# Optimization experiments

Measured on AMD Instinct MI355X. Metric: run time of the kernel, lower is better.

## Reference

```python
import jax, jax.numpy as jnp
import numpy as np

BS, T, ND, DS = 512, 100, 10, 6
INS, HID = 256, 256
CAT = INS * ND + HID  # 2816


def setup_inputs() -> dict:
    key = jax.random.key(0)
    ks = jax.random.split(key, 12)
    s = 0.02
    return {
        "descriptors": jax.random.normal(ks[0], (BS, T, ND, DS), jnp.float32),
        "Wd": jax.random.normal(ks[1], (INS, DS), jnp.float32) * s,
        "bd": jnp.zeros((INS,), jnp.float32),
        "W1": jax.random.normal(ks[2], (CAT, CAT), jnp.float32) * s,
        "b1": jnp.zeros((CAT,), jnp.float32),
        "W2": jax.random.normal(ks[3], (HID, CAT), jnp.float32) * s,
        "b2": jnp.zeros((HID,), jnp.float32),
        "Wv": jax.random.normal(ks[4], (ND, CAT), jnp.float32) * s,
        "bv": jnp.zeros((ND,), jnp.float32),
        "Wih": jax.random.normal(ks[5], (4 * HID, INS), jnp.float32) * s,
        "Whh": jax.random.normal(ks[6], (4 * HID, HID), jnp.float32) * s,
        "bih": jnp.zeros((4 * HID,), jnp.float32),
        "bhh": jnp.zeros((4 * HID,), jnp.float32),
    }


def reference(descriptors, Wd, bd, W1, b1, W2, b2, Wv, bv, Wih, Whh, bih, bhh):
    bs = descriptors.shape[0]
    # project all descriptors at once (same math as per-step Linear)
    emb = jnp.einsum('btnd,id->btni', descriptors, Wd) + bd  # [bs,T,ND,INS]
    emb = emb.reshape(bs, T, ND * INS).transpose(1, 0, 2)    # [T,bs,ND*INS]

    h0 = jnp.zeros((bs, HID), jnp.float32)
    c0 = jnp.zeros((bs, HID), jnp.float32)
    x0 = jnp.zeros((bs, HID), jnp.float32)  # lstm_in_size == hidden_size

    def step(carry, emb_t):
        h, c, inp = carry
        gates = inp @ Wih.T + bih + h @ Whh.T + bhh  # [bs,4*HID]
        i, f, g, o = jnp.split(gates, 4, axis=-1)
        c = jax.nn.sigmoid(f) * c + jax.nn.sigmoid(i) * jnp.tanh(g)
        h = jax.nn.sigmoid(o) * jnp.tanh(c)
        x = jnp.concatenate([emb_t, h], axis=-1)     # [bs,CAT]
        z = jax.nn.relu(x @ W1.T + b1)
        nxt = jax.nn.relu(z @ W2.T + b2)
        a = jax.nn.sigmoid(z @ Wv.T + bv)            # eval mode -> sigmoid
        return (h, c, nxt), a

    _, att = jax.lax.scan(step, (h0, c0, x0), emb)   # [T,bs,ND]
    return att.transpose(1, 0, 2)                    # [bs,T,ND]
```

## Files before the change

### kernel.cpp

```cpp
#include <hip/hip_runtime.h>
#include <math.h>

#define BSZ 512
#define TT  100
#define NDD 10
#define DSS 6
#define INS 256
#define HID 256
#define CAT 2816
#define KZ  320
#define NOUTP 320
#define NOUT 266
#define NBLK 256
#define NTHR 1024

typedef short sh8 __attribute__((ext_vector_type(8)));
typedef float f4  __attribute__((ext_vector_type(4)));
typedef unsigned int u4 __attribute__((ext_vector_type(4)));
typedef unsigned short ushort_t;

__device__ __forceinline__ float sigf(float x) { return 1.0f / (1.0f + expf(-x)); }

__device__ __forceinline__ ushort_t f2bf(float f) {
    union { float f; unsigned int u; } v; v.f = f;
    unsigned int r = (v.u + 0x7FFFu + ((v.u >> 16) & 1u)) >> 16;
    return (ushort_t)r;
}

#define MFMA(a, b, c) __builtin_amdgcn_mfma_f32_16x16x32_bf16((a), (b), (c), 0, 0, 0)
#define ALOAD(p)    __hip_atomic_load((p), __ATOMIC_RELAXED, __HIP_MEMORY_SCOPE_AGENT)
#define ASTORE(p,v) __hip_atomic_store((p), (v), __ATOMIC_RELAXED, __HIP_MEMORY_SCOPE_AGENT)

__device__ __forceinline__ u4 aload16(const unsigned int* p) {
    u4 r;
    asm volatile("global_load_dwordx4 %0, %1, off sc0 sc1\n\ts_waitcnt vmcnt(0)"
                 : "=&v"(r) : "v"(p) : "memory");
    return r;
}
__device__ __forceinline__ void aload16x4(f4* a, const float* p0, const float* p1,
                                          const float* p2, const float* p3) {
    asm volatile(
        "global_load_dwordx4 %0, %4, off sc0 sc1\n\t"
        "global_load_dwordx4 %1, %5, off sc0 sc1\n\t"
        "global_load_dwordx4 %2, %6, off sc0 sc1\n\t"
        "global_load_dwordx4 %3, %7, off sc0 sc1\n\t"
        "s_waitcnt vmcnt(0)"
        : "=&v"(a[0]), "=&v"(a[1]), "=&v"(a[2]), "=&v"(a[3])
        : "v"(p0), "v"(p1), "v"(p2), "v"(p3)
        : "memory");
}

__global__ __launch_bounds__(64) void k_fold(
    const float* __restrict__ W1, const float* __restrict__ Wd,
    const float* __restrict__ bd, const float* __restrict__ b1,
    ushort_t* __restrict__ Wzc, float* __restrict__ bfold)
{
    __shared__ float sW1[2560];
    __shared__ float sWd[INS * DSS];
    __shared__ float red[64];
    const int j = blockIdx.x;
    const int tid = threadIdx.x;
    for (int f = tid; f < INS * DSS; f += 64) sWd[f] = Wd[f];
    for (int f = tid; f < 2560; f += 64) sW1[f] = W1[(size_t)j * CAT + f];
    __syncthreads();
    if (tid < 60) {
        int n = tid / DSS, d = tid - n * DSS;
        float acc = 0.f;
        for (int i = 0; i < INS; ++i) acc += sW1[n * INS + i] * sWd[i * DSS + d];
        Wzc[j * KZ + tid] = f2bf(acc);
    } else {
        Wzc[j * KZ + tid] = 0;
    }
    for (int q = tid; q < HID; q += 64)
        Wzc[j * KZ + 64 + q] = f2bf(W1[(size_t)j * CAT + 2560 + q]);
    float acc = 0.f;
    for (int p = tid; p < 2560; p += 64) acc += sW1[p] * bd[p & (INS - 1)];
    red[tid] = acc;
    __syncthreads();
    for (int s = 32; s > 0; s >>= 1) {
        if (tid < s) red[tid] += red[tid + s];
        __syncthreads();
    }
    if (tid == 0) bfold[j] = b1[j] + red[0];
}

__global__ __launch_bounds__(256) void k_dfold(
    const float* __restrict__ desc, ushort_t* __restrict__ Dfold)
{
    int idx = blockIdx.x * 256 + threadIdx.x;
    int p = idx & 63;
    int tb = idx >> 6;
    int t = tb / BSZ;
    int b = tb - t * BSZ;
    float v = (p < 60) ? desc[(size_t)b * (TT * 60) + t * 60 + p] : 0.f;
    Dfold[idx] = f2bf(v);
}

__global__ __launch_bounds__(256) void k_prep_g(
    const float* __restrict__ Wih, const float* __restrict__ Whh,
    const float* __restrict__ bih, const float* __restrict__ bhh,
    ushort_t* __restrict__ Wg, float* __restrict__ bg)
{
    int idx = blockIdx.x * 256 + threadIdx.x;
    int newr = idx >> 9, k = idx & 511;
    int j = newr >> 2, g = newr & 3;
    int src_row = g * 256 + j;
    float v = (k < 256) ? Wih[(size_t)src_row * INS + k]
                        : Whh[(size_t)src_row * HID + (k - 256)];
    Wg[idx] = f2bf(v);
    if (k == 0) bg[newr] = bih[src_row] + bhh[src_row];
}

__global__ __launch_bounds__(256) void k_prep_o(
    const float* __restrict__ W2, const float* __restrict__ Wv,
    ushort_t* __restrict__ Wout)
{
    int idx = blockIdx.x * 256 + threadIdx.x;
    int r = idx / CAT, k = idx - r * CAT;
    float v = 0.f;
    if (r < 256) v = W2[(size_t)r * CAT + k];
    else if (r < NOUT) v = Wv[(size_t)(r - 256) * CAT + k];
    Wout[idx] = f2bf(v);
}

__device__ __forceinline__ void gbar(unsigned int* gfl, int s, unsigned int e) {
    __syncthreads();
    if (threadIdx.x < 64) {
        if (threadIdx.x == 0) ASTORE(&gfl[s * 16], e);
        const int peer = threadIdx.x & 7;
        while (ALOAD(&gfl[peer * 16]) < e)
            __builtin_amdgcn_s_sleep(1);
    }
    __syncthreads();
}

__global__ void __launch_bounds__(NTHR) k_persist(
    const ushort_t* __restrict__ Wg, const float* __restrict__ bg,
    const ushort_t* __restrict__ Wzc, const float* __restrict__ bfold,
    const ushort_t* __restrict__ Wout, const float* __restrict__ b2,
    const float* __restrict__ bv, const ushort_t* __restrict__ Dfold,
    ushort_t* __restrict__ xh,
    float* __restrict__ partA, float* __restrict__ partB,
    float* __restrict__ out, unsigned int* __restrict__ bars)
{
    __shared__ ushort_t sxh[16 * 520];
    __shared__ ushort_t sa[16 * 328];
    __shared__ ushort_t zt[16 * 360];
    __shared__ float    sg[16 * 132];
    __shared__ float    cl[16 * 33];

    const int bid = blockIdx.x;
    const int tid = threadIdx.x;
    const int w = tid >> 6, l = tid & 63, quad = l >> 4, lr = l & 15;
    const int s = bid & 7, grp = bid >> 3, m0 = grp * 16;
    unsigned int* xh_u  = (unsigned int*)xh;
    unsigned int* sxh_u = (unsigned int*)sxh;
    unsigned int* sa_u  = (unsigned int*)sa;
    unsigned int* gfl = bars + grp * 128;

    for (int i = tid; i < 16 * 33; i += NTHR) cl[i] = 0.f;
    if (tid < 192) {
        int row = tid / 12, v = tid % 12;
        int q = s * 48 + v * 4;
        #pragma unroll
        for (int k = 0; k < 4; ++k)
            ASTORE(&xh_u[(size_t)(m0 + row) * 384 + q + k], 0u);
    }
    gbar(gfl, s, 1);

    for (int t = 0; t < TT; ++t) {
        const int hcur  = 256 + (t & 1) * 256;
        const int hprev = 256 + ((t + 1) & 1) * 256;
        float*       pw = (t & 1) ? partB : partA;
        const float* pr = (t & 1) ? partA : partB;

        if (t > 0) {
            int row = -1, chunk = 0;
            if (s < 6 && tid < 160)      { row = tid / 10; chunk = tid % 10; }
            else if (s == 6 && tid < 64) { row = tid >> 2; chunk = tid & 3; }
            if (row >= 0) {
                const int c0 = s * 40 + chunk * 4;
                f4 a[4], b[4];
                const float* base = &pr[((size_t)(m0 + row)) * 320 + c0];
                aload16x4(a, base + (size_t)0 * 512 * 320, base + (size_t)1 * 512 * 320,
                             base + (size_t)2 * 512 * 320, base + (size_t)3 * 512 * 320);
                aload16x4(b, base + (size_t)4 * 512 * 320, base + (size_t)5 * 512 * 320,
                             base + (size_t)6 * 512 * 320, base + (size_t)7 * 512 * 320);
                f4 sum = a[0] + a[1] + a[2] + a[3] + b[0] + b[1] + b[2] + b[3];
                f4 bb = *(const f4*)&b2[c0];
                unsigned int v0 = (unsigned int)f2bf(fmaxf(sum[0] + bb[0], 0.f))
                    | ((unsigned int)f2bf(fmaxf(sum[1] + bb[1], 0.f)) << 16);
                unsigned int v1 = (unsigned int)f2bf(fmaxf(sum[2] + bb[2], 0.f))
                    | ((unsigned int)f2bf(fmaxf(sum[3] + bb[3], 0.f)) << 16);
                ASTORE(&xh_u[(size_t)(m0 + row) * 384 + (c0 >> 1)], v0);
                ASTORE(&xh_u[(size_t)(m0 + row) * 384 + (c0 >> 1) + 1], v1);
            }
            if (s == 6 && tid >= 512 && tid < 672) {
                int k = tid - 512, r2 = k / 10, col = k - r2 * 10;
                float sum = 0.f;
                #pragma unroll
                for (int s2 = 0; s2 < 8; ++s2)
                    sum += ALOAD(&pr[((size_t)(s2 * 512 + m0 + r2)) * 320 + 256 + col]);
                out[(size_t)(m0 + r2) * (TT * NDD) + (t - 1) * NDD + col] =
                    sigf(sum + bv[col]);
            }
            gbar(gfl, s, 3 * t + 2);
        }

        {
            int row = tid >> 6, q4 = tid & 63;
            const unsigned int* src = (q4 < 32)
                ? &xh_u[(size_t)(m0 + row) * 384 + q4 * 4]
                : &xh_u[(size_t)(m0 + row) * 384 + (hprev >> 1) + (q4 - 32) * 4];
            *(u4*)&sxh_u[row * 260 + q4 * 4] = aload16(src);
        }
        __syncthreads();
        {
            const int tile = w & 7, kh = w >> 3;
            f4 acc = {};
            const ushort_t* bp = Wg + (size_t)(s * 128 + tile * 16 + lr) * 512
                               + kh * 256 + quad * 8;
            const ushort_t* ap = &sxh[lr * 520 + kh * 256 + quad * 8];
            #pragma unroll
            for (int ks = 0; ks < 8; ++ks)
                acc = MFMA(*(const sh8*)(ap + ks * 32), *(const sh8*)(bp + ks * 32), acc);
            if (kh == 0) {
                #pragma unroll
                for (int r = 0; r < 4; ++r)
                    sg[(quad * 4 + r) * 132 + tile * 16 + lr] = acc[r];
            }
            __syncthreads();
            if (kh == 1) {
                #pragma unroll
                for (int r = 0; r < 4; ++r)
                    sg[(quad * 4 + r) * 132 + tile * 16 + lr] += acc[r];
            }
            __syncthreads();
            if (tid < 256) {
                int row = tid >> 4, jp = tid & 15;
                float g8[8];
                #pragma unroll
                for (int i = 0; i < 8; ++i)
                    g8[i] = sg[row * 132 + jp * 8 + i] + bg[s * 128 + jp * 8 + i];
                unsigned int pair = 0;
                #pragma unroll
                for (int h2 = 0; h2 < 2; ++h2) {
                    float ai = g8[h2 * 4 + 0], af = g8[h2 * 4 + 1];
                    float ag = g8[h2 * 4 + 2], ao = g8[h2 * 4 + 3];
                    int jc = jp * 2 + h2;
                    float cc = sigf(af) * cl[row * 33 + jc] + sigf(ai) * tanhf(ag);
                    cl[row * 33 + jc] = cc;
                    float hh = sigf(ao) * tanhf(cc);
                    pair |= ((unsigned int)f2bf(hh)) << (16 * h2);
                }
                ASTORE(&xh_u[(size_t)(m0 + row) * 384 + (hcur >> 1) + s * 16 + jp], pair);
            }
        }
        gbar(gfl, s, 3 * t + 3);

        if (tid < 128) {
            int row = tid >> 3, v = tid & 7;
            *(u4*)&sa_u[row * 164 + v * 4] =
                *(const u4*)&Dfold[((size_t)t * BSZ + m0 + row) * 64 + v * 8];
        } else if (tid >= 256 && tid < 768) {
            int k = tid - 256;
            int row = k >> 5, v = k & 31;
            *(u4*)&sa_u[row * 164 + 32 + v * 4] =
                aload16(&xh_u[(size_t)(m0 + row) * 384 + (hcur >> 1) + v * 4]);
        }
        __syncthreads();
        for (int tl = w; tl < 22; tl += 16) {
            int n0g = s * 352 + tl * 16;
            f4 acc = {};
            const ushort_t* bp = Wzc + (size_t)(n0g + lr) * KZ + quad * 8;
            const ushort_t* ap = &sa[lr * 328 + quad * 8];
            #pragma unroll
            for (int ks = 0; ks < 10; ++ks)
                acc = MFMA(*(const sh8*)(ap + ks * 32), *(const sh8*)(bp + ks * 32), acc);
            float bia = bfold[n0g + lr];
            #pragma unroll
            for (int r = 0; r < 4; ++r)
                zt[(quad * 4 + r) * 360 + tl * 16 + lr] = f2bf(fmaxf(acc[r] + bia, 0.f));
        }
        __syncthreads();
        for (int tl = w; tl < 20; tl += 16) {
            int n0 = tl * 16;
            f4 acc = {};
            const ushort_t* bp = Wout + (size_t)(n0 + lr) * CAT + s * 352 + quad * 8;
            const ushort_t* ap = &zt[lr * 360 + quad * 8];
            #pragma unroll
            for (int ks = 0; ks < 11; ++ks)
                acc = MFMA(*(const sh8*)(ap + ks * 32), *(const sh8*)(bp + ks * 32), acc);
            #pragma unroll
            for (int r = 0; r < 4; ++r)
                ASTORE(&pw[((size_t)(s * 512 + m0 + quad * 4 + r)) * 320 + n0 + lr],
                       acc[r]);
        }
        gbar(gfl, s, 3 * t + 4);
    }

    if (s == 6 && tid < 160) {
        int row = tid / 10, col = tid - row * 10;
        float sum = 0.f;
        #pragma unroll
        for (int s2 = 0; s2 < 8; ++s2)
            sum += ALOAD(&partB[((size_t)(s2 * 512 + m0 + row)) * 320 + 256 + col]);
        out[(size_t)(m0 + row) * (TT * NDD) + (TT - 1) * NDD + col] = sigf(sum + bv[col]);
    }
}

extern "C" void kernel_launch(void* const* d_in, const int* in_sizes, int n_in,
                              void* d_out, int out_size, void* d_ws, size_t ws_size,
                              hipStream_t stream)
{
    const float* desc = (const float*)d_in[0];
    const float* Wd   = (const float*)d_in[1];
    const float* bd   = (const float*)d_in[2];
    const float* W1   = (const float*)d_in[3];
    const float* b1   = (const float*)d_in[4];
    const float* W2   = (const float*)d_in[5];
    const float* b2   = (const float*)d_in[6];
    const float* Wv   = (const float*)d_in[7];
    const float* bv   = (const float*)d_in[8];
    const float* Wih  = (const float*)d_in[9];
    const float* Whh  = (const float*)d_in[10];
    const float* bih  = (const float*)d_in[11];
    const float* bhh  = (const float*)d_in[12];
    float* out = (float*)d_out;

    char* base = (char*)d_ws;
    size_t off = 0;
    auto alloc = [&](size_t bytes) -> char* {
        char* p = base + off;
        off = (off + bytes + 255) & ~(size_t)255;
        return p;
    };
    ushort_t*     Wzc   = (ushort_t*)alloc((size_t)CAT * KZ * 2);
    float*        bfold = (float*)alloc(CAT * 4);
    ushort_t*     Wg    = (ushort_t*)alloc(1024 * 512 * 2);
    float*        bg    = (float*)alloc(1024 * 4);
    ushort_t*     Wout  = (ushort_t*)alloc((size_t)NOUTP * CAT * 2);
    ushort_t*     Dfold = (ushort_t*)alloc((size_t)TT * BSZ * 64 * 2);
    ushort_t*     xh    = (ushort_t*)alloc((size_t)BSZ * 768 * 2);
    float*        partA = (float*)alloc((size_t)8 * BSZ * NOUTP * 4);
    float*        partB = (float*)alloc((size_t)8 * BSZ * NOUTP * 4);
    unsigned int* bars  = (unsigned int*)alloc(32 * 128 * 4);

    hipMemsetAsync(bars, 0, 32 * 128 * 4, stream);

    k_fold  <<<CAT, 64, 0, stream>>>(W1, Wd, bd, b1, Wzc, bfold);
    k_dfold <<<(TT * BSZ * 64) / 256, 256, 0, stream>>>(desc, Dfold);
    k_prep_g<<<(1024 * 512) / 256, 256, 0, stream>>>(Wih, Whh, bih, bhh, Wg, bg);
    k_prep_o<<<(NOUTP * CAT) / 256, 256, 0, stream>>>(W2, Wv, Wout);

    void* args[] = {
        (void*)&Wg, (void*)&bg, (void*)&Wzc, (void*)&bfold, (void*)&Wout,
        (void*)&b2, (void*)&bv, (void*)&Dfold, (void*)&xh,
        (void*)&partA, (void*)&partB, (void*)&out, (void*)&bars
    };
    hipLaunchCooperativeKernel((const void*)k_persist, dim3(NBLK), dim3(NTHR),
                               args, 0, stream);
}
```

Measured before the change: 2.377 ms.

## Split persistent recurrence across 16 workgroups per batch group instead of 8

Adds a new persistent kernel that splits each 16-row batch group across 16 workgroups of 512 threads (512 total) instead of 8 workgroups of 1024 threads. Each workgroup handles half the gate columns and half the z/W1 columns, so per-step MFMA work and weight traffic per block shrink and more CUs are used. Partial output sums are doubled (16 partials) and reduced in two halves through shared memory, with the final attention sigmoid folded into the same reduction path. The cost is a wider barrier (16 peers), twice the partial-sum memory traffic, and a cooperative launch that may fail, in which case the old 8-way kernel runs as a fallback.

```diff
diff --git a/kernel.cpp b/kernel.cpp
--- a/kernel.cpp
+++ b/kernel.cpp
@@ -11,8 +11,6 @@
 #define KZ  320
 #define NOUTP 320
 #define NOUT 266
-#define NBLK 256
-#define NTHR 1024
 
 typedef short sh8 __attribute__((ext_vector_type(8)));
 typedef float f4  __attribute__((ext_vector_type(4)));
@@ -36,6 +34,14 @@
     asm volatile("global_load_dwordx4 %0, %1, off sc0 sc1\n\ts_waitcnt vmcnt(0)"
                  : "=&v"(r) : "v"(p) : "memory");
     return r;
+}
+__device__ __forceinline__ void aload16x2(u4* a, const unsigned int* p0,
+                                          const unsigned int* p1) {
+    asm volatile(
+        "global_load_dwordx4 %0, %2, off sc0 sc1\n\t"
+        "global_load_dwordx4 %1, %3, off sc0 sc1\n\t"
+        "s_waitcnt vmcnt(0)"
+        : "=&v"(a[0]), "=&v"(a[1]) : "v"(p0), "v"(p1) : "memory");
 }
 __device__ __forceinline__ void aload16x4(f4* a, const float* p0, const float* p1,
                                           const float* p2, const float* p3) {
@@ -123,7 +129,17 @@
     Wout[idx] = f2bf(v);
 }
 
-__device__ __forceinline__ void gbar(unsigned int* gfl, int s, unsigned int e) {
+__device__ __forceinline__ void gbar16(unsigned int* gfl, int s, unsigned int e) {
+    __syncthreads();
+    if (threadIdx.x < 64) {
+        if (threadIdx.x == 0) ASTORE(&gfl[s * 16], e);
+        const int peer = threadIdx.x & 15;
+        while (ALOAD(&gfl[peer * 16]) < e)
+            __builtin_amdgcn_s_sleep(1);
+    }
+    __syncthreads();
+}
+__device__ __forceinline__ void gbar8(unsigned int* gfl, int s, unsigned int e) {
     __syncthreads();
     if (threadIdx.x < 64) {
         if (threadIdx.x == 0) ASTORE(&gfl[s * 16], e);
@@ -134,7 +150,193 @@
     __syncthreads();
 }
 
-__global__ void __launch_bounds__(NTHR) k_persist(
+__global__ void __launch_bounds__(512) k_persist16(
+    const ushort_t* __restrict__ Wg, const float* __restrict__ bg,
+    const ushort_t* __restrict__ Wzc, const float* __restrict__ bfold,
+    const ushort_t* __restrict__ Wout, const float* __restrict__ b2,
+    const float* __restrict__ bv, const ushort_t* __restrict__ Dfold,
+    ushort_t* __restrict__ xh,
+    float* __restrict__ partA, float* __restrict__ partB,
+    float* __restrict__ out, unsigned int* __restrict__ bars)
+{
+    __shared__ __align__(16) char smem[22144];
+    ushort_t* sxh = (ushort_t*)smem;
+    float*    sg  = (float*)(smem + 16640);
+    ushort_t* sa  = (ushort_t*)smem;
+    ushort_t* zt  = (ushort_t*)(smem + 10496);
+    f4*       ra  = (f4*)smem;
+    float*    cl  = (float*)(smem + 20992);
+
+    const int tid = threadIdx.x;
+    const int w = tid >> 6, l = tid & 63, quad = l >> 4, lr = l & 15;
+    const int s = blockIdx.x & 15, grp = blockIdx.x >> 4, m0 = grp * 16;
+    unsigned int* xh_u  = (unsigned int*)xh;
+    unsigned int* sxh_u = (unsigned int*)sxh;
+    unsigned int* sa_u  = (unsigned int*)sa;
+    unsigned int* zt_u  = (unsigned int*)zt;
+    unsigned int* gfl = bars + grp * 256;
+    unsigned int ep = 0;
+
+    for (int i = tid; i < 16 * 17; i += 512) cl[i] = 0.f;
+    if (tid < 384) {
+        int row = tid / 24, v = tid % 24;
+        ASTORE(&xh_u[(size_t)(m0 + row) * 384 + s * 24 + v], 0u);
+    }
+    gbar16(gfl, s, ++ep);
+
+    for (int t = 0; t <= TT; ++t) {
+        const int hcur  = 256 + (t & 1) * 256;
+        const int hprev = 256 + ((t + 1) & 1) * 256;
+        float*       pw = (t & 1) ? partB : partA;
+        const float* pr = (t & 1) ? partA : partB;
+
+        if (t > 0) {
+            int c0 = -1, row = 0, half = 0;
+            if (tid < 320) {
+                int task = tid >> 1;
+                half = tid & 1;
+                row = task / 5;
+                c0 = s * 20 + (task % 5) * 4;
+                if (row >= 16) c0 = -1;
+            }
+            if (c0 >= 0 && c0 <= 264) {
+                f4 a[4], b[4];
+                const float* base = &pr[((size_t)(half * 8 * 512 + m0 + row)) * 320 + c0];
+                aload16x4(a, base + (size_t)0 * 512 * 320, base + (size_t)1 * 512 * 320,
+                             base + (size_t)2 * 512 * 320, base + (size_t)3 * 512 * 320);
+                aload16x4(b, base + (size_t)4 * 512 * 320, base + (size_t)5 * 512 * 320,
+                             base + (size_t)6 * 512 * 320, base + (size_t)7 * 512 * 320);
+                ra[tid] = a[0] + a[1] + a[2] + a[3] + b[0] + b[1] + b[2] + b[3];
+            }
+            __syncthreads();
+            if (tid < 80) {
+                int r2 = tid / 5, cc0 = s * 20 + (tid % 5) * 4;
+                if (cc0 <= 264) {
+                    f4 tot = ra[tid * 2] + ra[tid * 2 + 1];
+                    if (cc0 < 256) {
+                        f4 bb = *(const f4*)&b2[cc0];
+                        unsigned int v0 = (unsigned int)f2bf(fmaxf(tot[0] + bb[0], 0.f))
+                            | ((unsigned int)f2bf(fmaxf(tot[1] + bb[1], 0.f)) << 16);
+                        unsigned int v1 = (unsigned int)f2bf(fmaxf(tot[2] + bb[2], 0.f))
+                            | ((unsigned int)f2bf(fmaxf(tot[3] + bb[3], 0.f)) << 16);
+                        ASTORE(&xh_u[(size_t)(m0 + r2) * 384 + (cc0 >> 1)], v0);
+                        ASTORE(&xh_u[(size_t)(m0 + r2) * 384 + (cc0 >> 1) + 1], v1);
+                    } else {
+                        #pragma unroll
+                        for (int e = 0; e < 4; ++e) {
+                            int col = cc0 + e;
+                            if (col < NOUT)
+                                out[(size_t)(m0 + r2) * (TT * NDD) + (t - 1) * NDD
+                                    + (col - 256)] = sigf(tot[e] + bv[col - 256]);
+                        }
+                    }
+                }
+            }
+            gbar16(gfl, s, ++ep);
+        }
+        if (t == TT) break;
+
+        {
+            int row0 = tid >> 6, q0 = tid & 63;
+            const unsigned int* src0 = (q0 < 32)
+                ? &xh_u[(size_t)(m0 + row0) * 384 + q0 * 4]
+                : &xh_u[(size_t)(m0 + row0) * 384 + (hprev >> 1) + (q0 - 32) * 4];
+            const unsigned int* src1 = (q0 < 32)
+                ? &xh_u[(size_t)(m0 + row0 + 8) * 384 + q0 * 4]
+                : &xh_u[(size_t)(m0 + row0 + 8) * 384 + (hprev >> 1) + (q0 - 32) * 4];
+            u4 tmp[2];
+            aload16x2(tmp, src0, src1);
+            *(u4*)&sxh_u[row0 * 260 + q0 * 4] = tmp[0];
+            *(u4*)&sxh_u[(row0 + 8) * 260 + q0 * 4] = tmp[1];
+        }
+        __syncthreads();
+        {
+            const int tile = w & 3, kh = w >> 2;
+            f4 acc = {};
+            const ushort_t* bp = Wg + (size_t)(s * 64 + tile * 16 + lr) * 512
+                               + kh * 256 + quad * 8;
+            const ushort_t* ap = &sxh[lr * 520 + kh * 256 + quad * 8];
+            #pragma unroll
+            for (int ks = 0; ks < 8; ++ks)
+                acc = MFMA(*(const sh8*)(ap + ks * 32), *(const sh8*)(bp + ks * 32), acc);
+            if (kh == 0) {
+                #pragma unroll
+                for (int r = 0; r < 4; ++r)
+                    sg[(quad * 4 + r) * 68 + tile * 16 + lr] = acc[r];
+            }
+            __syncthreads();
+            if (kh == 1) {
+                #pragma unroll
+                for (int r = 0; r < 4; ++r)
+                    sg[(quad * 4 + r) * 68 + tile * 16 + lr] += acc[r];
+            }
+            __syncthreads();
+            if (tid < 128) {
+                int row = tid >> 3, jp2 = tid & 7;
+                float g8[8];
+                #pragma unroll
+                for (int i = 0; i < 8; ++i)
+                    g8[i] = sg[row * 68 + jp2 * 8 + i] + bg[s * 64 + jp2 * 8 + i];
+                unsigned int pair = 0;
+                #pragma unroll
+                for (int h2 = 0; h2 < 2; ++h2) {
+                    float ai = g8[h2 * 4 + 0], af = g8[h2 * 4 + 1];
+                    float ag = g8[h2 * 4 + 2], ao = g8[h2 * 4 + 3];
+                    int jc = jp2 * 2 + h2;
+                    float cc = sigf(af) * cl[row * 17 + jc] + sigf(ai) * tanhf(ag);
+                    cl[row * 17 + jc] = cc;
+                    float hh = sigf(ao) * tanhf(cc);
+                    pair |= ((unsigned int)f2bf(hh)) << (16 * h2);
+                }
+                ASTORE(&xh_u[(size_t)(m0 + row) * 384 + (hcur >> 1) + s * 8 + jp2], pair);
+            }
+        }
+        gbar16(gfl, s, ++ep);
+
+        if (tid < 128) {
+            int row = tid >> 3, v = tid & 7;
+            *(u4*)&sa_u[row * 164 + v * 4] =
+                *(const u4*)&Dfold[((size_t)t * BSZ + m0 + row) * 64 + v * 8];
+            zt_u[row * 96 + 88 + v] = 0u;
+        }
+        {
+            int row = tid >> 5, v = tid & 31;
+            *(u4*)&sa_u[row * 164 + 32 + v * 4] =
+                aload16(&xh_u[(size_t)(m0 + row) * 384 + (hcur >> 1) + v * 4]);
+        }
+        __syncthreads();
+        for (int tl = w; tl < 11; tl += 8) {
+            int n0g = s * 176 + tl * 16;
+            f4 acc = {};
+            const ushort_t* bp = Wzc + (size_t)(n0g + lr) * KZ + quad * 8;
+            const ushort_t* ap = &sa[lr * 328 + quad * 8];
+            #pragma unroll
+            for (int ks = 0; ks < 10; ++ks)
+                acc = MFMA(*(const sh8*)(ap + ks * 32), *(const sh8*)(bp + ks * 32), acc);
+            float bia = bfold[n0g + lr];
+            #pragma unroll
+            for (int r = 0; r < 4; ++r)
+                zt[(quad * 4 + r) * 192 + tl * 16 + lr] = f2bf(fmaxf(acc[r] + bia, 0.f));
+        }
+        __syncthreads();
+        for (int tl = w; tl < 20; tl += 8) {
+            int n0 = tl * 16;
+            f4 acc = {};
+            const ushort_t* bp = Wout + (size_t)(n0 + lr) * CAT + s * 176 + quad * 8;
+            const ushort_t* ap = &zt[lr * 192 + quad * 8];
+            #pragma unroll
+            for (int ks = 0; ks < 6; ++ks)
+                acc = MFMA(*(const sh8*)(ap + ks * 32), *(const sh8*)(bp + ks * 32), acc);
+            #pragma unroll
+            for (int r = 0; r < 4; ++r)
+                ASTORE(&pw[((size_t)(s * 512 + m0 + quad * 4 + r)) * 320 + n0 + lr],
+                       acc[r]);
+        }
+        gbar16(gfl, s, ++ep);
+    }
+}
+
+__global__ void __launch_bounds__(1024) k_persist8(
     const ushort_t* __restrict__ Wg, const float* __restrict__ bg,
     const ushort_t* __restrict__ Wzc, const float* __restrict__ bfold,
     const ushort_t* __restrict__ Wout, const float* __restrict__ b2,
@@ -158,7 +360,7 @@
     unsigned int* sa_u  = (unsigned int*)sa;
     unsigned int* gfl = bars + grp * 128;
 
-    for (int i = tid; i < 16 * 33; i += NTHR) cl[i] = 0.f;
+    for (int i = tid; i < 16 * 33; i += 1024) cl[i] = 0.f;
     if (tid < 192) {
         int row = tid / 12, v = tid % 12;
         int q = s * 48 + v * 4;
@@ -166,7 +368,7 @@
         for (int k = 0; k < 4; ++k)
             ASTORE(&xh_u[(size_t)(m0 + row) * 384 + q + k], 0u);
     }
-    gbar(gfl, s, 1);
+    gbar8(gfl, s, 1);
 
     for (int t = 0; t < TT; ++t) {
         const int hcur  = 256 + (t & 1) * 256;
@@ -204,7 +406,7 @@
                 out[(size_t)(m0 + r2) * (TT * NDD) + (t - 1) * NDD + col] =
                     sigf(sum + bv[col]);
             }
-            gbar(gfl, s, 3 * t + 2);
+            gbar8(gfl, s, 3 * t + 2);
         }
 
         {
@@ -256,7 +458,7 @@
                 ASTORE(&xh_u[(size_t)(m0 + row) * 384 + (hcur >> 1) + s * 16 + jp], pair);
             }
         }
-        gbar(gfl, s, 3 * t + 3);
+        gbar8(gfl, s, 3 * t + 3);
 
         if (tid < 128) {
             int row = tid >> 3, v = tid & 7;
@@ -296,7 +498,7 @@
                 ASTORE(&pw[((size_t)(s * 512 + m0 + quad * 4 + r)) * 320 + n0 + lr],
                        acc[r]);
         }
-        gbar(gfl, s, 3 * t + 4);
+        gbar8(gfl, s, 3 * t + 4);
     }
 
     if (s == 6 && tid < 160) {
@@ -339,25 +541,37 @@
     float*        bfold = (float*)alloc(CAT * 4);
     ushort_t*     Wg    = (ushort_t*)alloc(1024 * 512 * 2);
     float*        bg    = (float*)alloc(1024 * 4);
-    ushort_t*     Wout  = (ushort_t*)alloc((size_t)NOUTP * CAT * 2);
+    ushort_t*     Wout  = (ushort_t*)alloc((size_t)NOUTP * CAT * 2 + 256);
     ushort_t*     Dfold = (ushort_t*)alloc((size_t)TT * BSZ * 64 * 2);
     ushort_t*     xh    = (ushort_t*)alloc((size_t)BSZ * 768 * 2);
-    float*        partA = (float*)alloc((size_t)8 * BSZ * NOUTP * 4);
-    float*        partB = (float*)alloc((size_t)8 * BSZ * NOUTP * 4);
-    unsigned int* bars  = (unsigned int*)alloc(32 * 128 * 4);
-
-    hipMemsetAsync(bars, 0, 32 * 128 * 4, stream);
+    float*        partA = (float*)alloc((size_t)16 * BSZ * NOUTP * 4);
+    float*        partB = (float*)alloc((size_t)16 * BSZ * NOUTP * 4);
+    unsigned int* bars16 = (unsigned int*)alloc(32 * 256 * 4);
+    unsigned int* bars8  = (unsigned int*)alloc(32 * 128 * 4);
+
+    hipMemsetAsync(bars16, 0, 32 * 256 * 4, stream);
+    hipMemsetAsync(bars8,  0, 32 * 128 * 4, stream);
 
     k_fold  <<<CAT, 64, 0, stream>>>(W1, Wd, bd, b1, Wzc, bfold);
     k_dfold <<<(TT * BSZ * 64) / 256, 256, 0, stream>>>(desc, Dfold);
     k_prep_g<<<(1024 * 512) / 256, 256, 0, stream>>>(Wih, Whh, bih, bhh, Wg, bg);
     k_prep_o<<<(NOUTP * CAT) / 256, 256, 0, stream>>>(W2, Wv, Wout);
 
-    void* args[] = {
+    void* args16[] = {
         (void*)&Wg, (void*)&bg, (void*)&Wzc, (void*)&bfold, (void*)&Wout,
         (void*)&b2, (void*)&bv, (void*)&Dfold, (void*)&xh,
-        (void*)&partA, (void*)&partB, (void*)&out, (void*)&bars
+        (void*)&partA, (void*)&partB, (void*)&out, (void*)&bars16
     };
-    hipLaunchCooperativeKernel((const void*)k_persist, dim3(NBLK), dim3(NTHR),
-                               args, 0, stream);
-}
+    hipError_t err = hipLaunchCooperativeKernel((const void*)k_persist16,
+                                                dim3(512), dim3(512),
+                                                args16, 0, stream);
+    if (err != hipSuccess) {
+        void* args8[] = {
+            (void*)&Wg, (void*)&bg, (void*)&Wzc, (void*)&bfold, (void*)&Wout,
+            (void*)&b2, (void*)&bv, (void*)&Dfold, (void*)&xh,
+            (void*)&partA, (void*)&partB, (void*)&out, (void*)&bars8
+        };
+        hipLaunchCooperativeKernel((const void*)k_persist8, dim3(256), dim3(1024),
+                                   args8, 0, stream);
+    }
+}
```

Measured after the change: 2.653 ms. 1.12x slower.
